# Performance work log

Hardware: AMD Instinct MI355X
Metric: run time of the kernel (lower is better)

The kernel has to match this reference:

```python
import jax, jax.numpy as jnp
import numpy as np

T, H, I, E, K = 4096, 2048, 1408, 8, 2  # tokens, hidden, intermediate, experts, top_k


def setup_inputs() -> dict:
    key = jax.random.key(0)
    ks = jax.random.split(key, 6)
    hidden_states = jax.random.normal(ks[0], (T, H), dtype=jnp.float32)
    gate_weight = jax.random.normal(ks[1], (E, H), dtype=jnp.float32) * 0.02  # fp32 gate, per source assert
    w13_weight = jax.random.randint(ks[2], (E, 2 * I, H), -127, 128, dtype=jnp.int8)
    w13_weight_scale = jax.random.uniform(ks[3], (E, 2 * I), dtype=jnp.float32, minval=0.5, maxval=1.5) * 0.005
    w2_weight = jax.random.randint(ks[4], (E, H, I), -127, 128, dtype=jnp.int8)
    w2_weight_scale = jax.random.uniform(ks[5], (E, H), dtype=jnp.float32, minval=0.5, maxval=1.5) * 0.005
    return dict(hidden_states=hidden_states, gate_weight=gate_weight,
                w13_weight=w13_weight, w13_weight_scale=w13_weight_scale,
                w2_weight=w2_weight, w2_weight_scale=w2_weight_scale)


def _dynamic_quant_i8(x):
    # per-token dynamic symmetric int8: scale = max|x|/127 (smooth scales default to ones)
    s = jnp.maximum(jnp.max(jnp.abs(x), axis=-1, keepdims=True) / 127.0, 1e-8)
    q = jnp.clip(jnp.round(x / s), -127.0, 127.0)
    return q, s


def reference(hidden_states, gate_weight, w13_weight, w13_weight_scale, w2_weight, w2_weight_scale):
    # --- gating: fp32 linear + topk softmax (renormalize=True) ---
    logits = hidden_states @ gate_weight.T              # [T, E]
    probs = jax.nn.softmax(logits, axis=-1)
    topv, topi = jax.lax.top_k(probs, K)                # [T, K]
    gates = topv / jnp.sum(topv, axis=-1, keepdims=True)
    # dense routing weights [T, E]: gate value where expert selected, else 0
    route = jnp.zeros((T, E), hidden_states.dtype).at[jnp.arange(T)[:, None], topi].add(gates)

    # --- dynamic per-token int8 quant of routed input (same token value for each of its K copies) ---
    q_in, s_in = _dynamic_quant_i8(hidden_states)       # [T, H], [T, 1]

    # --- grouped w8a8 GEMM (fc1) -> SwiGLU -> requant -> grouped GEMM (fc2) -> weighted combine ---
    def step(acc, xs):
        w13, s13, w2, s2w, r = xs                       # per-expert weights / route column [T]
        h1 = (q_in @ w13.T.astype(jnp.float32)) * s_in * s13[None, :]   # dequant fc1: [T, 2I]
        g, u = h1[:, :I], h1[:, I:]
        act = jax.nn.silu(g) * u                        # SwiGLU
        q_a, s_a = _dynamic_quant_i8(act)
        h2 = (q_a @ w2.T.astype(jnp.float32)) * s_a * s2w[None, :]      # dequant fc2: [T, H]
        return acc + r[:, None] * h2, None

    acc0 = jnp.zeros_like(hidden_states)
    out, _ = jax.lax.scan(step, acc0,
                          (w13_weight, w13_weight_scale, w2_weight, w2_weight_scale, route.T))
    return out
```

## Files before the change

kernel.cpp:

```cpp
#include <hip/hip_runtime.h>

#define T_TOK 4096
#define H_DIM 2048
#define I_DIM 1408
#define E_NUM 8
#define NI2   (2 * I_DIM)

typedef int v4i __attribute__((ext_vector_type(4)));

#define GLD_LDS16(gptr, lptr)                                                        \
  __builtin_amdgcn_global_load_lds(                                                  \
      (const __attribute__((address_space(1))) void*)(gptr),                         \
      (__attribute__((address_space(3))) void*)(lptr), 16, 0, 0)

__global__ __launch_bounds__(256) void pack_i8(const int* __restrict__ src,
                                               signed char* __restrict__ dst,
                                               int n16) {
  int i = blockIdx.x * 256 + threadIdx.x;
  if (i >= n16) return;
  const int4* s4 = (const int4*)src + (size_t)i * 4;
  int4 v0 = s4[0], v1 = s4[1], v2 = s4[2], v3 = s4[3];
  union { signed char c[16]; int4 v; } pk;
  pk.c[0] = (signed char)v0.x;  pk.c[1] = (signed char)v0.y;
  pk.c[2] = (signed char)v0.z;  pk.c[3] = (signed char)v0.w;
  pk.c[4] = (signed char)v1.x;  pk.c[5] = (signed char)v1.y;
  pk.c[6] = (signed char)v1.z;  pk.c[7] = (signed char)v1.w;
  pk.c[8] = (signed char)v2.x;  pk.c[9] = (signed char)v2.y;
  pk.c[10] = (signed char)v2.z; pk.c[11] = (signed char)v2.w;
  pk.c[12] = (signed char)v3.x; pk.c[13] = (signed char)v3.y;
  pk.c[14] = (signed char)v3.z; pk.c[15] = (signed char)v3.w;
  ((int4*)dst)[i] = pk.v;
}

__global__ __launch_bounds__(256) void gate_route_quant(
    const float* __restrict__ hs, const float* __restrict__ gw,
    signed char* __restrict__ qin, float* __restrict__ s_in,
    int* __restrict__ tok_list, int* __restrict__ cnt,
    int* __restrict__ epos, float* __restrict__ gts) {
  const int t = blockIdx.x;
  const int tid = threadIdx.x;
  const int lane = tid & 63;
  const int wave = tid >> 6;
  const float* row = hs + (size_t)t * H_DIM;

  const float4* r4 = (const float4*)row + tid * 2;
  float4 xa = r4[0], xb = r4[1];
  float x[8] = {xa.x, xa.y, xa.z, xa.w, xb.x, xb.y, xb.z, xb.w};

  double pd[8];
  for (int e = 0; e < 8; e++) pd[e] = 0.0;
  float am = 0.f;
  for (int j = 0; j < 8; j++) {
    float v = x[j];
    am = fmaxf(am, fabsf(v));
    int col = tid * 8 + j;
    for (int e = 0; e < 8; e++)
      pd[e] += (double)v * (double)gw[e * H_DIM + col];
  }
  for (int e = 0; e < 8; e++)
    for (int s = 32; s; s >>= 1) pd[e] += __shfl_down(pd[e], s);
  for (int s = 32; s; s >>= 1) am = fmaxf(am, __shfl_down(am, s));

  __shared__ double sred[4][8];
  __shared__ float sam[4];
  __shared__ float sbc;
  if (lane == 0) {
    for (int e = 0; e < 8; e++) sred[wave][e] = pd[e];
    sam[wave] = am;
  }
  __syncthreads();
  if (tid == 0) {
    float l[8];
    for (int e = 0; e < 8; e++)
      l[e] = (float)(sred[0][e] + sred[1][e] + sred[2][e] + sred[3][e]);
    float amx = fmaxf(fmaxf(sam[0], sam[1]), fmaxf(sam[2], sam[3]));
    float s = fmaxf(amx / 127.0f, 1e-8f);
    s_in[t] = s;
    sbc = s;
    int i1 = 0;
    for (int e = 1; e < 8; e++) if (l[e] > l[i1]) i1 = e;
    int i2 = -1;
    for (int e = 0; e < 8; e++) {
      if (e == i1) continue;
      if (i2 < 0 || l[e] > l[i2]) i2 = e;
    }
    float d = expf(l[i2] - l[i1]);
    float g1 = 1.0f / (1.0f + d);
    float g2 = d / (1.0f + d);
    int p1 = atomicAdd(&cnt[i1], 1);
    tok_list[i1 * T_TOK + p1] = t;
    int p2 = atomicAdd(&cnt[i2], 1);
    tok_list[i2 * T_TOK + p2] = t;
    epos[2 * t] = (i1 << 16) | p1;     gts[2 * t] = g1;
    epos[2 * t + 1] = (i2 << 16) | p2; gts[2 * t + 1] = g2;
  }
  __syncthreads();
  float s = sbc;
  union { signed char c[8]; unsigned long long u; } pk;
  for (int j = 0; j < 8; j++) {
    float q = rintf(x[j] / s);
    q = fminf(127.f, fmaxf(-127.f, q));
    pk.c[j] = (signed char)q;
  }
  ((unsigned long long*)(qin + (size_t)t * H_DIM))[tid] = pk.u;
}

__global__ void calc_off(const int* __restrict__ cnt, int* __restrict__ off) {
  if (threadIdx.x == 0) {
    int s = 0;
    for (int e = 0; e < E_NUM; e++) { off[e] = s; s += cnt[e]; }
  }
}

__global__ __launch_bounds__(256, 2) void gemm1_silu(
    const signed char* __restrict__ qw13, const signed char* __restrict__ qin,
    const float* __restrict__ s_in, const float* __restrict__ s13,
    const int* __restrict__ tok_list, const int* __restrict__ cnt,
    const int* __restrict__ off, float* __restrict__ act,
    unsigned int* __restrict__ amax) {
  const int e = blockIdx.z;
  const int ce = cnt[e];
  const int m0 = blockIdx.y * 128;
  if (m0 >= ce) return;
  const int n0 = blockIdx.x * 128;

  __shared__ __align__(16) signed char As[128 * 64];
  __shared__ __align__(16) signed char Bg[128 * 64];
  __shared__ __align__(16) signed char Bu[128 * 64];

  const int tid = threadIdx.x;
  const int lane = tid & 63;
  const int wave = tid >> 6;
  const int quad = lane >> 4;
  const int ln = lane & 15;
  const int wm = wave & 1;
  const int wn = wave >> 1;

  const int* tl = tok_list + e * T_TOK;
  const int rowA0 = tid >> 2;
  const int rowA1 = rowA0 + 64;
  const int kc = ((tid ^ (tid >> 4)) & 3) * 16;

  const int tA0 = tl[min(m0 + rowA0, ce - 1)];
  const int tA1 = tl[min(m0 + rowA1, ce - 1)];
  const signed char* gA0 = qin + (size_t)tA0 * H_DIM + kc;
  const signed char* gA1 = qin + (size_t)tA1 * H_DIM + kc;
  const signed char* w13e = qw13 + (size_t)e * NI2 * H_DIM;
  const signed char* gBg0 = w13e + (size_t)(n0 + rowA0) * H_DIM + kc;
  const signed char* gBg1 = w13e + (size_t)(n0 + rowA1) * H_DIM + kc;
  const signed char* gBu0 = gBg0 + (size_t)I_DIM * H_DIM;
  const signed char* gBu1 = gBg1 + (size_t)I_DIM * H_DIM;
  const int lds0 = (tid & ~63) * 16;
  const int lds1 = 4096 + lds0;

  const int rq0 = ((quad ^ (ln >> 2)) & 3) * 16;

  v4i accg[4][4], accu[4][4];
  v4i zero = {0, 0, 0, 0};
#pragma unroll
  for (int i = 0; i < 4; i++)
#pragma unroll
    for (int j = 0; j < 4; j++) { accg[i][j] = zero; accu[i][j] = zero; }

  for (int k0 = 0; k0 < H_DIM; k0 += 64) {
    __syncthreads();
    GLD_LDS16(gA0 + k0, As + lds0);
    GLD_LDS16(gA1 + k0, As + lds1);
    GLD_LDS16(gBg0 + k0, Bg + lds0);
    GLD_LDS16(gBg1 + k0, Bg + lds1);
    GLD_LDS16(gBu0 + k0, Bu + lds0);
    GLD_LDS16(gBu1 + k0, Bu + lds1);
    __syncthreads();

    v4i af[4], bgf[4], buf_[4];
#pragma unroll
    for (int mt = 0; mt < 4; mt++)
      af[mt] = *(const v4i*)(As + (wm * 64 + mt * 16 + ln) * 64 + rq0);
#pragma unroll
    for (int nt = 0; nt < 4; nt++) {
      bgf[nt] = *(const v4i*)(Bg + (wn * 64 + nt * 16 + ln) * 64 + rq0);
      buf_[nt] = *(const v4i*)(Bu + (wn * 64 + nt * 16 + ln) * 64 + rq0);
    }
#pragma unroll
    for (int mt = 0; mt < 4; mt++)
#pragma unroll
      for (int nt = 0; nt < 4; nt++) {
        accg[mt][nt] = __builtin_amdgcn_mfma_i32_16x16x64_i8(af[mt], bgf[nt], accg[mt][nt], 0, 0, 0);
        accu[mt][nt] = __builtin_amdgcn_mfma_i32_16x16x64_i8(af[mt], buf_[nt], accu[mt][nt], 0, 0, 0);
      }
  }

  const float* s13e = s13 + e * NI2;
  float sg[4], su[4];
  int ncol[4];
#pragma unroll
  for (int nt = 0; nt < 4; nt++) {
    int n = n0 + wn * 64 + nt * 16 + ln;
    ncol[nt] = n;
    sg[nt] = s13e[n];
    su[nt] = s13e[I_DIM + n];
  }
  const int offe = off[e];
#pragma unroll
  for (int mt = 0; mt < 4; mt++) {
#pragma unroll
    for (int r = 0; r < 4; r++) {
      int mrel = m0 + wm * 64 + mt * 16 + quad * 4 + r;
      bool valid = mrel < ce;
      int tok = tl[valid ? mrel : 0];
      float si = s_in[tok];
      int crow = offe + mrel;
      float* arow = act + (size_t)crow * I_DIM;
      float am = 0.f;
#pragma unroll
      for (int nt = 0; nt < 4; nt++) {
        float g = (float)accg[mt][nt][r] * si * sg[nt];
        float u = (float)accu[mt][nt][r] * si * su[nt];
        float a = g / (1.0f + expf(-g)) * u;
        if (valid) arow[ncol[nt]] = a;
        am = fmaxf(am, fabsf(a));
      }
      for (int s = 1; s < 16; s <<= 1) am = fmaxf(am, __shfl_xor(am, s, 16));
      if (valid && ln == 0) atomicMax(amax + crow, __float_as_uint(am));
    }
  }
}

__global__ __launch_bounds__(256) void quant_act(const float* __restrict__ act,
                                                 const unsigned int* __restrict__ amax,
                                                 signed char* __restrict__ qa,
                                                 float* __restrict__ s_a) {
  const int r = blockIdx.x;
  float am = __uint_as_float(amax[r]);
  float s = fmaxf(am / 127.0f, 1e-8f);
  if (threadIdx.x == 0) s_a[r] = s;
  const float* arow = act + (size_t)r * I_DIM;
  signed char* qrow = qa + (size_t)r * I_DIM;
  for (int j = threadIdx.x; j < I_DIM; j += 256) {
    float q = rintf(arow[j] / s);
    q = fminf(127.f, fmaxf(-127.f, q));
    qrow[j] = (signed char)q;
  }
}

__global__ __launch_bounds__(256, 3) void gemm2_h2(
    const signed char* __restrict__ qw2, const signed char* __restrict__ qa,
    const float* __restrict__ s_a, const float* __restrict__ s2w,
    const int* __restrict__ cnt, const int* __restrict__ off,
    float* __restrict__ h2s) {
  const int e = blockIdx.z;
  const int ce = cnt[e];
  const int m0 = blockIdx.y * 128;
  if (m0 >= ce) return;
  const int n0 = blockIdx.x * 128;
  const int offe = off[e];

  __shared__ __align__(16) signed char As[128 * 64];
  __shared__ __align__(16) signed char Bs[128 * 64];

  const int tid = threadIdx.x;
  const int lane = tid & 63;
  const int wave = tid >> 6;
  const int quad = lane >> 4;
  const int ln = lane & 15;
  const int wm = wave & 1;
  const int wn = wave >> 1;

  const int rowA0 = tid >> 2;
  const int rowA1 = rowA0 + 64;
  const int kc = ((tid ^ (tid >> 4)) & 3) * 16;

  const signed char* gA0 = qa + (size_t)(offe + min(m0 + rowA0, ce - 1)) * I_DIM + kc;
  const signed char* gA1 = qa + (size_t)(offe + min(m0 + rowA1, ce - 1)) * I_DIM + kc;
  const signed char* w2e = qw2 + (size_t)e * H_DIM * I_DIM;
  const signed char* gB0 = w2e + (size_t)(n0 + rowA0) * I_DIM + kc;
  const signed char* gB1 = w2e + (size_t)(n0 + rowA1) * I_DIM + kc;
  const int lds0 = (tid & ~63) * 16;
  const int lds1 = 4096 + lds0;
  const int rq0 = ((quad ^ (ln >> 2)) & 3) * 16;

  v4i acc[4][4];
  v4i zero = {0, 0, 0, 0};
#pragma unroll
  for (int i = 0; i < 4; i++)
#pragma unroll
    for (int j = 0; j < 4; j++) acc[i][j] = zero;

  for (int k0 = 0; k0 < I_DIM; k0 += 64) {
    __syncthreads();
    GLD_LDS16(gA0 + k0, As + lds0);
    GLD_LDS16(gA1 + k0, As + lds1);
    GLD_LDS16(gB0 + k0, Bs + lds0);
    GLD_LDS16(gB1 + k0, Bs + lds1);
    __syncthreads();

    v4i af[4], bf[4];
#pragma unroll
    for (int mt = 0; mt < 4; mt++)
      af[mt] = *(const v4i*)(As + (wm * 64 + mt * 16 + ln) * 64 + rq0);
#pragma unroll
    for (int nt = 0; nt < 4; nt++)
      bf[nt] = *(const v4i*)(Bs + (wn * 64 + nt * 16 + ln) * 64 + rq0);
#pragma unroll
    for (int mt = 0; mt < 4; mt++)
#pragma unroll
      for (int nt = 0; nt < 4; nt++)
        acc[mt][nt] = __builtin_amdgcn_mfma_i32_16x16x64_i8(af[mt], bf[nt], acc[mt][nt], 0, 0, 0);
  }

  const float* s2e = s2w + e * H_DIM;
  float sw[4];
  int ncol[4];
#pragma unroll
  for (int nt = 0; nt < 4; nt++) {
    int n = n0 + wn * 64 + nt * 16 + ln;
    ncol[nt] = n;
    sw[nt] = s2e[n];
  }
#pragma unroll
  for (int mt = 0; mt < 4; mt++) {
#pragma unroll
    for (int r = 0; r < 4; r++) {
      int mrel = m0 + wm * 64 + mt * 16 + quad * 4 + r;
      if (mrel >= ce) continue;
      float sa = s_a[offe + mrel];
      float* orow = h2s + (size_t)(offe + mrel) * H_DIM;
#pragma unroll
      for (int nt = 0; nt < 4; nt++)
        orow[ncol[nt]] = (float)acc[mt][nt][r] * sa * sw[nt];
    }
  }
}

__global__ __launch_bounds__(256) void gather_out(
    const float* __restrict__ h2s, const int* __restrict__ epos,
    const float* __restrict__ gts, const int* __restrict__ off,
    float* __restrict__ out) {
  const int t = blockIdx.x;
  int a = epos[2 * t], b = epos[2 * t + 1];
  float g1 = gts[2 * t], g2 = gts[2 * t + 1];
  int r1 = off[a >> 16] + (a & 0xffff);
  int r2 = off[b >> 16] + (b & 0xffff);
  const float4* R1 = (const float4*)(h2s + (size_t)r1 * H_DIM);
  const float4* R2 = (const float4*)(h2s + (size_t)r2 * H_DIM);
  float4* O = (float4*)(out + (size_t)t * H_DIM);
  for (int c = threadIdx.x; c < H_DIM / 4; c += 256) {
    float4 x = R1[c], y = R2[c];
    float4 z;
    z.x = g1 * x.x + g2 * y.x;
    z.y = g1 * x.y + g2 * y.y;
    z.z = g1 * x.z + g2 * y.z;
    z.w = g1 * x.w + g2 * y.w;
    O[c] = z;
  }
}

extern "C" void kernel_launch(void* const* d_in, const int* in_sizes, int n_in,
                              void* d_out, int out_size, void* d_ws, size_t ws_size,
                              hipStream_t stream) {
  const float* hs = (const float*)d_in[0];
  const float* gw = (const float*)d_in[1];
  const int* w13 = (const int*)d_in[2];
  const float* s13 = (const float*)d_in[3];
  const int* w2 = (const int*)d_in[4];
  const float* s2w = (const float*)d_in[5];
  float* out = (float*)d_out;

  char* ws = (char*)d_ws;
  size_t o = 0;
  auto take = [&](size_t b) {
    char* p = ws + o;
    o += (b + 255) & ~(size_t)255;
    return p;
  };
  signed char* qw13 = (signed char*)take((size_t)E_NUM * NI2 * H_DIM);
  signed char* qin = (signed char*)take((size_t)T_TOK * H_DIM);
  float* act = (float*)take((size_t)T_TOK * 2 * I_DIM * 4);
  float* h2s = (float*)qw13;
  signed char* qw2 = (signed char*)take((size_t)E_NUM * H_DIM * I_DIM);
  signed char* qa = (signed char*)take((size_t)T_TOK * 2 * I_DIM);
  float* sin_ = (float*)take((size_t)T_TOK * 4);
  float* sa = (float*)take((size_t)T_TOK * 2 * 4);
  unsigned int* amax = (unsigned int*)take((size_t)T_TOK * 2 * 4);
  int* tokl = (int*)take((size_t)E_NUM * T_TOK * 4);
  int* epos = (int*)take((size_t)T_TOK * 2 * 4);
  float* gts = (float*)take((size_t)T_TOK * 2 * 4);
  int* cnt = (int*)take(E_NUM * 4);
  int* off = (int*)take(E_NUM * 4);

  hipMemsetAsync(cnt, 0, E_NUM * 4, stream);
  hipMemsetAsync(amax, 0, (size_t)T_TOK * 2 * 4, stream);

  {
    int n16 = E_NUM * NI2 * H_DIM / 16;
    pack_i8<<<(n16 + 255) / 256, 256, 0, stream>>>(w13, qw13, n16);
  }
  {
    int n16 = E_NUM * H_DIM * I_DIM / 16;
    pack_i8<<<(n16 + 255) / 256, 256, 0, stream>>>(w2, qw2, n16);
  }
  gate_route_quant<<<T_TOK, 256, 0, stream>>>(hs, gw, qin, sin_, tokl, cnt, epos, gts);
  calc_off<<<1, 64, 0, stream>>>(cnt, off);
  {
    dim3 g(I_DIM / 128, T_TOK / 128, E_NUM);
    gemm1_silu<<<g, 256, 0, stream>>>(qw13, qin, sin_, s13, tokl, cnt, off, act, amax);
  }
  quant_act<<<T_TOK * 2, 256, 0, stream>>>(act, amax, qa, sa);
  {
    dim3 g(H_DIM / 128, T_TOK / 128, E_NUM);
    gemm2_h2<<<g, 256, 0, stream>>>(qw2, qa, sa, s2w, cnt, off, h2s);
  }
  gather_out<<<T_TOK, 256, 0, stream>>>(h2s, epos, gts, off, out);
}
```

Measured before the change: 635.2 us.

## Shrink GEMM M-tiles to 64, deterministic expert lists, merge weight pack kernels

The gating kernel no longer uses global atomics. It now writes each token's top-2 expert ids, and a new per-expert kernel builds ordered token lists with a ballot/popcount prefix scan, which makes row order deterministic. Both grouped GEMMs move from 128x128 to 64x128 tiles, with each wave covering 32 columns, and take higher occupancy bounds. This gives more blocks and less padding waste on uneven expert counts, at the cost of lower per-block reuse of the weights. The two int8 weight-packing launches are merged into one, and the XOR LDS swizzle is dropped, which may add bank conflicts.

```diff
diff --git a/kernel.cpp b/kernel.cpp
--- a/kernel.cpp
+++ b/kernel.cpp
@@ -13,12 +13,19 @@
       (const __attribute__((address_space(1))) void*)(gptr),                         \
       (__attribute__((address_space(3))) void*)(lptr), 16, 0, 0)
 
-__global__ __launch_bounds__(256) void pack_i8(const int* __restrict__ src,
-                                               signed char* __restrict__ dst,
-                                               int n16) {
+__global__ __launch_bounds__(256) void pack_all(const int* __restrict__ w13,
+                                                const int* __restrict__ w2,
+                                                signed char* __restrict__ qw13,
+                                                signed char* __restrict__ qw2,
+                                                int n16a, int n16tot) {
   int i = blockIdx.x * 256 + threadIdx.x;
-  if (i >= n16) return;
-  const int4* s4 = (const int4*)src + (size_t)i * 4;
+  if (i >= n16tot) return;
+  const int* src;
+  signed char* dst;
+  int j;
+  if (i < n16a) { src = w13; dst = qw13; j = i; }
+  else          { src = w2;  dst = qw2;  j = i - n16a; }
+  const int4* s4 = (const int4*)src + (size_t)j * 4;
   int4 v0 = s4[0], v1 = s4[1], v2 = s4[2], v3 = s4[3];
   union { signed char c[16]; int4 v; } pk;
   pk.c[0] = (signed char)v0.x;  pk.c[1] = (signed char)v0.y;
@@ -29,14 +36,13 @@
   pk.c[10] = (signed char)v2.z; pk.c[11] = (signed char)v2.w;
   pk.c[12] = (signed char)v3.x; pk.c[13] = (signed char)v3.y;
   pk.c[14] = (signed char)v3.z; pk.c[15] = (signed char)v3.w;
-  ((int4*)dst)[i] = pk.v;
+  ((int4*)dst)[j] = pk.v;
 }
 
 __global__ __launch_bounds__(256) void gate_route_quant(
     const float* __restrict__ hs, const float* __restrict__ gw,
     signed char* __restrict__ qin, float* __restrict__ s_in,
-    int* __restrict__ tok_list, int* __restrict__ cnt,
-    int* __restrict__ epos, float* __restrict__ gts) {
+    int* __restrict__ tope, float* __restrict__ gts) {
   const int t = blockIdx.x;
   const int tid = threadIdx.x;
   const int lane = tid & 63;
@@ -85,14 +91,8 @@
       if (i2 < 0 || l[e] > l[i2]) i2 = e;
     }
     float d = expf(l[i2] - l[i1]);
-    float g1 = 1.0f / (1.0f + d);
-    float g2 = d / (1.0f + d);
-    int p1 = atomicAdd(&cnt[i1], 1);
-    tok_list[i1 * T_TOK + p1] = t;
-    int p2 = atomicAdd(&cnt[i2], 1);
-    tok_list[i2 * T_TOK + p2] = t;
-    epos[2 * t] = (i1 << 16) | p1;     gts[2 * t] = g1;
-    epos[2 * t + 1] = (i2 << 16) | p2; gts[2 * t + 1] = g2;
+    tope[2 * t] = i1;     gts[2 * t] = 1.0f / (1.0f + d);
+    tope[2 * t + 1] = i2; gts[2 * t + 1] = d / (1.0f + d);
   }
   __syncthreads();
   float s = sbc;
@@ -105,6 +105,41 @@
   ((unsigned long long*)(qin + (size_t)t * H_DIM))[tid] = pk.u;
 }
 
+__global__ __launch_bounds__(256) void build_lists(
+    const int* __restrict__ tope, int* __restrict__ tok_list,
+    int* __restrict__ epos, int* __restrict__ cnt) {
+  const int e = blockIdx.x;
+  const int tid = threadIdx.x;
+  const int lane = tid & 63;
+  const int wave = tid >> 6;
+  __shared__ int wsum[4];
+  __shared__ int base_s;
+  if (tid == 0) base_s = 0;
+  __syncthreads();
+  for (int t0 = 0; t0 < T_TOK; t0 += 256) {
+    int t = t0 + tid;
+    int i1 = tope[2 * t], i2 = tope[2 * t + 1];
+    int slot = (i1 == e) ? 0 : ((i2 == e) ? 1 : -1);
+    unsigned long long m = __ballot(slot >= 0);
+    int wpre = __popcll(m & ((1ull << lane) - 1ull));
+    if (lane == 0) wsum[wave] = __popcll(m);
+    __syncthreads();
+    int pre = wpre;
+    for (int w = 0; w < wave; w++) pre += wsum[w];
+    int total = wsum[0] + wsum[1] + wsum[2] + wsum[3];
+    int b = base_s;
+    if (slot >= 0) {
+      int pos = b + pre;
+      tok_list[e * T_TOK + pos] = t;
+      epos[2 * t + slot] = (e << 16) | pos;
+    }
+    __syncthreads();
+    if (tid == 0) base_s = b + total;
+  }
+  __syncthreads();
+  if (tid == 0) cnt[e] = base_s;
+}
+
 __global__ void calc_off(const int* __restrict__ cnt, int* __restrict__ off) {
   if (threadIdx.x == 0) {
     int s = 0;
@@ -112,7 +147,7 @@
   }
 }
 
-__global__ __launch_bounds__(256, 2) void gemm1_silu(
+__global__ __launch_bounds__(256, 3) void gemm1_silu(
     const signed char* __restrict__ qw13, const signed char* __restrict__ qin,
     const float* __restrict__ s_in, const float* __restrict__ s13,
     const int* __restrict__ tok_list, const int* __restrict__ cnt,
@@ -120,11 +155,11 @@
     unsigned int* __restrict__ amax) {
   const int e = blockIdx.z;
   const int ce = cnt[e];
-  const int m0 = blockIdx.y * 128;
+  const int m0 = blockIdx.y * 64;
   if (m0 >= ce) return;
   const int n0 = blockIdx.x * 128;
 
-  __shared__ __align__(16) signed char As[128 * 64];
+  __shared__ __align__(16) signed char As[64 * 64];
   __shared__ __align__(16) signed char Bg[128 * 64];
   __shared__ __align__(16) signed char Bu[128 * 64];
 
@@ -133,69 +168,61 @@
   const int wave = tid >> 6;
   const int quad = lane >> 4;
   const int ln = lane & 15;
-  const int wm = wave & 1;
-  const int wn = wave >> 1;
 
   const int* tl = tok_list + e * T_TOK;
-  const int rowA0 = tid >> 2;
-  const int rowA1 = rowA0 + 64;
-  const int kc = ((tid ^ (tid >> 4)) & 3) * 16;
-
-  const int tA0 = tl[min(m0 + rowA0, ce - 1)];
-  const int tA1 = tl[min(m0 + rowA1, ce - 1)];
-  const signed char* gA0 = qin + (size_t)tA0 * H_DIM + kc;
-  const signed char* gA1 = qin + (size_t)tA1 * H_DIM + kc;
+  const int rowA = tid >> 2;
+  const int kc = (tid & 3) * 16;
+
+  const int tA = tl[min(m0 + rowA, ce - 1)];
+  const signed char* gA = qin + (size_t)tA * H_DIM + kc;
   const signed char* w13e = qw13 + (size_t)e * NI2 * H_DIM;
-  const signed char* gBg0 = w13e + (size_t)(n0 + rowA0) * H_DIM + kc;
-  const signed char* gBg1 = w13e + (size_t)(n0 + rowA1) * H_DIM + kc;
+  const signed char* gBg0 = w13e + (size_t)(n0 + rowA) * H_DIM + kc;
+  const signed char* gBg1 = w13e + (size_t)(n0 + rowA + 64) * H_DIM + kc;
   const signed char* gBu0 = gBg0 + (size_t)I_DIM * H_DIM;
   const signed char* gBu1 = gBg1 + (size_t)I_DIM * H_DIM;
-  const int lds0 = (tid & ~63) * 16;
-  const int lds1 = 4096 + lds0;
-
-  const int rq0 = ((quad ^ (ln >> 2)) & 3) * 16;
-
-  v4i accg[4][4], accu[4][4];
+  const int ldsA = tid * 16;
+  const int lds1 = 4096 + ldsA;
+
+  v4i accg[4][2], accu[4][2];
   v4i zero = {0, 0, 0, 0};
 #pragma unroll
   for (int i = 0; i < 4; i++)
 #pragma unroll
-    for (int j = 0; j < 4; j++) { accg[i][j] = zero; accu[i][j] = zero; }
+    for (int j = 0; j < 2; j++) { accg[i][j] = zero; accu[i][j] = zero; }
 
   for (int k0 = 0; k0 < H_DIM; k0 += 64) {
     __syncthreads();
-    GLD_LDS16(gA0 + k0, As + lds0);
-    GLD_LDS16(gA1 + k0, As + lds1);
-    GLD_LDS16(gBg0 + k0, Bg + lds0);
+    GLD_LDS16(gA + k0, As + ldsA);
+    GLD_LDS16(gBg0 + k0, Bg + ldsA);
     GLD_LDS16(gBg1 + k0, Bg + lds1);
-    GLD_LDS16(gBu0 + k0, Bu + lds0);
+    GLD_LDS16(gBu0 + k0, Bu + ldsA);
     GLD_LDS16(gBu1 + k0, Bu + lds1);
     __syncthreads();
 
-    v4i af[4], bgf[4], buf_[4];
+    v4i af[4], bgf[2], buf_[2];
 #pragma unroll
     for (int mt = 0; mt < 4; mt++)
-      af[mt] = *(const v4i*)(As + (wm * 64 + mt * 16 + ln) * 64 + rq0);
-#pragma unroll
-    for (int nt = 0; nt < 4; nt++) {
-      bgf[nt] = *(const v4i*)(Bg + (wn * 64 + nt * 16 + ln) * 64 + rq0);
-      buf_[nt] = *(const v4i*)(Bu + (wn * 64 + nt * 16 + ln) * 64 + rq0);
+      af[mt] = *(const v4i*)(As + (mt * 16 + ln) * 64 + quad * 16);
+#pragma unroll
+    for (int nt = 0; nt < 2; nt++) {
+      bgf[nt] = *(const v4i*)(Bg + (wave * 32 + nt * 16 + ln) * 64 + quad * 16);
+      buf_[nt] = *(const v4i*)(Bu + (wave * 32 + nt * 16 + ln) * 64 + quad * 16);
     }
 #pragma unroll
     for (int mt = 0; mt < 4; mt++)
 #pragma unroll
-      for (int nt = 0; nt < 4; nt++) {
+      for (int nt = 0; nt < 2; nt++) {
         accg[mt][nt] = __builtin_amdgcn_mfma_i32_16x16x64_i8(af[mt], bgf[nt], accg[mt][nt], 0, 0, 0);
         accu[mt][nt] = __builtin_amdgcn_mfma_i32_16x16x64_i8(af[mt], buf_[nt], accu[mt][nt], 0, 0, 0);
       }
   }
 
   const float* s13e = s13 + e * NI2;
-  float sg[4], su[4];
-  int ncol[4];
-#pragma unroll
-  for (int nt = 0; nt < 4; nt++) {
-    int n = n0 + wn * 64 + nt * 16 + ln;
+  float sg[2], su[2];
+  int ncol[2];
+#pragma unroll
+  for (int nt = 0; nt < 2; nt++) {
+    int n = n0 + wave * 32 + nt * 16 + ln;
     ncol[nt] = n;
     sg[nt] = s13e[n];
     su[nt] = s13e[I_DIM + n];
@@ -205,7 +232,7 @@
   for (int mt = 0; mt < 4; mt++) {
 #pragma unroll
     for (int r = 0; r < 4; r++) {
-      int mrel = m0 + wm * 64 + mt * 16 + quad * 4 + r;
+      int mrel = m0 + mt * 16 + quad * 4 + r;
       bool valid = mrel < ce;
       int tok = tl[valid ? mrel : 0];
       float si = s_in[tok];
@@ -213,7 +240,7 @@
       float* arow = act + (size_t)crow * I_DIM;
       float am = 0.f;
 #pragma unroll
-      for (int nt = 0; nt < 4; nt++) {
+      for (int nt = 0; nt < 2; nt++) {
         float g = (float)accg[mt][nt][r] * si * sg[nt];
         float u = (float)accu[mt][nt][r] * si * su[nt];
         float a = g / (1.0f + expf(-g)) * u;
@@ -243,19 +270,19 @@
   }
 }
 
-__global__ __launch_bounds__(256, 3) void gemm2_h2(
+__global__ __launch_bounds__(256, 4) void gemm2_h2(
     const signed char* __restrict__ qw2, const signed char* __restrict__ qa,
     const float* __restrict__ s_a, const float* __restrict__ s2w,
     const int* __restrict__ cnt, const int* __restrict__ off,
     float* __restrict__ h2s) {
   const int e = blockIdx.z;
   const int ce = cnt[e];
-  const int m0 = blockIdx.y * 128;
+  const int m0 = blockIdx.y * 64;
   if (m0 >= ce) return;
   const int n0 = blockIdx.x * 128;
   const int offe = off[e];
 
-  __shared__ __align__(16) signed char As[128 * 64];
+  __shared__ __align__(16) signed char As[64 * 64];
   __shared__ __align__(16) signed char Bs[128 * 64];
 
   const int tid = threadIdx.x;
@@ -263,57 +290,51 @@
   const int wave = tid >> 6;
   const int quad = lane >> 4;
   const int ln = lane & 15;
-  const int wm = wave & 1;
-  const int wn = wave >> 1;
-
-  const int rowA0 = tid >> 2;
-  const int rowA1 = rowA0 + 64;
-  const int kc = ((tid ^ (tid >> 4)) & 3) * 16;
-
-  const signed char* gA0 = qa + (size_t)(offe + min(m0 + rowA0, ce - 1)) * I_DIM + kc;
-  const signed char* gA1 = qa + (size_t)(offe + min(m0 + rowA1, ce - 1)) * I_DIM + kc;
+
+  const int rowA = tid >> 2;
+  const int kc = (tid & 3) * 16;
+
+  const signed char* gA = qa + (size_t)(offe + min(m0 + rowA, ce - 1)) * I_DIM + kc;
   const signed char* w2e = qw2 + (size_t)e * H_DIM * I_DIM;
-  const signed char* gB0 = w2e + (size_t)(n0 + rowA0) * I_DIM + kc;
-  const signed char* gB1 = w2e + (size_t)(n0 + rowA1) * I_DIM + kc;
-  const int lds0 = (tid & ~63) * 16;
-  const int lds1 = 4096 + lds0;
-  const int rq0 = ((quad ^ (ln >> 2)) & 3) * 16;
-
-  v4i acc[4][4];
+  const signed char* gB0 = w2e + (size_t)(n0 + rowA) * I_DIM + kc;
+  const signed char* gB1 = w2e + (size_t)(n0 + rowA + 64) * I_DIM + kc;
+  const int ldsA = tid * 16;
+  const int lds1 = 4096 + ldsA;
+
+  v4i acc[4][2];
   v4i zero = {0, 0, 0, 0};
 #pragma unroll
   for (int i = 0; i < 4; i++)
 #pragma unroll
-    for (int j = 0; j < 4; j++) acc[i][j] = zero;
+    for (int j = 0; j < 2; j++) acc[i][j] = zero;
 
   for (int k0 = 0; k0 < I_DIM; k0 += 64) {
     __syncthreads();
-    GLD_LDS16(gA0 + k0, As + lds0);
-    GLD_LDS16(gA1 + k0, As + lds1);
-    GLD_LDS16(gB0 + k0, Bs + lds0);
+    GLD_LDS16(gA + k0, As + ldsA);
+    GLD_LDS16(gB0 + k0, Bs + ldsA);
     GLD_LDS16(gB1 + k0, Bs + lds1);
     __syncthreads();
 
-    v4i af[4], bf[4];
+    v4i af[4], bf[2];
 #pragma unroll
     for (int mt = 0; mt < 4; mt++)
-      af[mt] = *(const v4i*)(As + (wm * 64 + mt * 16 + ln) * 64 + rq0);
-#pragma unroll
-    for (int nt = 0; nt < 4; nt++)
-      bf[nt] = *(const v4i*)(Bs + (wn * 64 + nt * 16 + ln) * 64 + rq0);
+      af[mt] = *(const v4i*)(As + (mt * 16 + ln) * 64 + quad * 16);
+#pragma unroll
+    for (int nt = 0; nt < 2; nt++)
+      bf[nt] = *(const v4i*)(Bs + (wave * 32 + nt * 16 + ln) * 64 + quad * 16);
 #pragma unroll
     for (int mt = 0; mt < 4; mt++)
 #pragma unroll
-      for (int nt = 0; nt < 4; nt++)
+      for (int nt = 0; nt < 2; nt++)
         acc[mt][nt] = __builtin_amdgcn_mfma_i32_16x16x64_i8(af[mt], bf[nt], acc[mt][nt], 0, 0, 0);
   }
 
   const float* s2e = s2w + e * H_DIM;
-  float sw[4];
-  int ncol[4];
-#pragma unroll
-  for (int nt = 0; nt < 4; nt++) {
-    int n = n0 + wn * 64 + nt * 16 + ln;
+  float sw[2];
+  int ncol[2];
+#pragma unroll
+  for (int nt = 0; nt < 2; nt++) {
+    int n = n0 + wave * 32 + nt * 16 + ln;
     ncol[nt] = n;
     sw[nt] = s2e[n];
   }
@@ -321,12 +342,12 @@
   for (int mt = 0; mt < 4; mt++) {
 #pragma unroll
     for (int r = 0; r < 4; r++) {
-      int mrel = m0 + wm * 64 + mt * 16 + quad * 4 + r;
+      int mrel = m0 + mt * 16 + quad * 4 + r;
       if (mrel >= ce) continue;
       float sa = s_a[offe + mrel];
       float* orow = h2s + (size_t)(offe + mrel) * H_DIM;
 #pragma unroll
-      for (int nt = 0; nt < 4; nt++)
+      for (int nt = 0; nt < 2; nt++)
         orow[ncol[nt]] = (float)acc[mt][nt][r] * sa * sw[nt];
     }
   }
@@ -383,31 +404,30 @@
   float* sa = (float*)take((size_t)T_TOK * 2 * 4);
   unsigned int* amax = (unsigned int*)take((size_t)T_TOK * 2 * 4);
   int* tokl = (int*)take((size_t)E_NUM * T_TOK * 4);
+  int* tope = (int*)take((size_t)T_TOK * 2 * 4);
   int* epos = (int*)take((size_t)T_TOK * 2 * 4);
   float* gts = (float*)take((size_t)T_TOK * 2 * 4);
   int* cnt = (int*)take(E_NUM * 4);
   int* off = (int*)take(E_NUM * 4);
 
-  hipMemsetAsync(cnt, 0, E_NUM * 4, stream);
   hipMemsetAsync(amax, 0, (size_t)T_TOK * 2 * 4, stream);
 
   {
-    int n16 = E_NUM * NI2 * H_DIM / 16;
-    pack_i8<<<(n16 + 255) / 256, 256, 0, stream>>>(w13, qw13, n16);
-  }
-  {
-    int n16 = E_NUM * H_DIM * I_DIM / 16;
-    pack_i8<<<(n16 + 255) / 256, 256, 0, stream>>>(w2, qw2, n16);
-  }
-  gate_route_quant<<<T_TOK, 256, 0, stream>>>(hs, gw, qin, sin_, tokl, cnt, epos, gts);
+    int n16a = E_NUM * NI2 * H_DIM / 16;
+    int n16b = E_NUM * H_DIM * I_DIM / 16;
+    int n16tot = n16a + n16b;
+    pack_all<<<(n16tot + 255) / 256, 256, 0, stream>>>(w13, w2, qw13, qw2, n16a, n16tot);
+  }
+  gate_route_quant<<<T_TOK, 256, 0, stream>>>(hs, gw, qin, sin_, tope, gts);
+  build_lists<<<E_NUM, 256, 0, stream>>>(tope, tokl, epos, cnt);
   calc_off<<<1, 64, 0, stream>>>(cnt, off);
   {
-    dim3 g(I_DIM / 128, T_TOK / 128, E_NUM);
+    dim3 g(I_DIM / 128, T_TOK / 64, E_NUM);
     gemm1_silu<<<g, 256, 0, stream>>>(qw13, qin, sin_, s13, tokl, cnt, off, act, amax);
   }
   quant_act<<<T_TOK * 2, 256, 0, stream>>>(act, amax, qa, sa);
   {
-    dim3 g(H_DIM / 128, T_TOK / 128, E_NUM);
+    dim3 g(H_DIM / 128, T_TOK / 64, E_NUM);
     gemm2_h2<<<g, 256, 0, stream>>>(qw2, qa, sa, s2w, cnt, off, h2s);
   }
   gather_out<<<T_TOK, 256, 0, stream>>>(h2s, epos, gts, off, out);
```

After: 584.1 us. -8.0%, faster.
